# Kernel optimization log

Hardware: AMD Instinct MI355X
Metric: run time of the kernel (lower is better)

## Reference

```python
import jax, jax.numpy as jnp
import numpy as np

SIGMA = 1e-4
GAMMA = 1e-4
BG_COLOR = (1.0, 1.0, 1.0)
ZNEAR = 1.0
ZFAR = 100.0
EPS = 1e-10


def setup_inputs() -> dict:
    key = jax.random.key(0)
    ks = jax.random.split(key, 7)
    N, H, W, K = 4, 512, 512, 8
    F, V = 100000, 50000
    p2f = jax.random.randint(ks[0], (N, H, W, K), 0, F)
    bg = jax.random.uniform(ks[1], (N, H, W, K)) < 0.3
    pix_to_face = jnp.where(bg, -1, p2f)
    b = jax.random.uniform(ks[2], (N, H, W, K, 3)) + 1e-3
    bary_coords = b / b.sum(-1, keepdims=True)  # valid barycentric weights
    dists = jax.random.normal(ks[3], (N, H, W, K)) * 1e-4  # signed edge distances
    zbuf = ZNEAR + (ZFAR - ZNEAR) * jax.random.uniform(ks[4], (N, H, W, K))
    zbuf = jnp.sort(zbuf, axis=-1)  # rasterizer returns K faces sorted by depth
    faces = jax.random.randint(ks[5], (F, 3), 0, V)
    vn = jax.random.normal(ks[6], (V, 3))
    vertex_normals = vn / jnp.linalg.norm(vn, axis=-1, keepdims=True)
    return dict(pix_to_face=pix_to_face, bary_coords=bary_coords, dists=dists,
                zbuf=zbuf, faces=faces, vertex_normals=vertex_normals)


def reference(pix_to_face, bary_coords, dists, zbuf, faces, vertex_normals):
    # ---- interpolate_face_attributes ----
    mask = pix_to_face >= 0                              # (N,H,W,K)
    idx = jnp.where(mask, pix_to_face, 0)
    face_normals = vertex_normals[faces]                 # (F,3,3) gather verts per face
    attrs = face_normals[idx]                            # (N,H,W,K,3,3) irregular gather
    pixel_normals = jnp.einsum('nhwkv,nhwkvc->nhwkc', bary_coords, attrs)
    pixel_normals = jnp.where(mask[..., None], pixel_normals, 0.0)

    # ---- softmax_rgb_blend ----
    maskf = mask.astype(pixel_normals.dtype)
    prob_map = jax.nn.sigmoid(-dists / SIGMA) * maskf
    alpha = 1.0 - jnp.prod(1.0 - prob_map, axis=-1)      # (N,H,W)
    z_inv = (ZFAR - zbuf) / (ZFAR - ZNEAR) * maskf
    z_inv_max = jnp.maximum(jnp.max(z_inv, axis=-1, keepdims=True), EPS)
    weights_num = prob_map * jnp.exp((z_inv - z_inv_max) / GAMMA)
    delta = jnp.maximum(jnp.exp((EPS - z_inv_max[..., 0]) / GAMMA), EPS)  # (N,H,W)
    denom = weights_num.sum(-1) + delta                  # (N,H,W)
    weighted_colors = jnp.einsum('nhwk,nhwkc->nhwc', weights_num, pixel_normals)
    bg = jnp.asarray(BG_COLOR, dtype=pixel_normals.dtype)
    rgb = (weighted_colors + delta[..., None] * bg) / denom[..., None]
    return jnp.concatenate([rgb, alpha[..., None]], axis=-1)  # (N,H,W,4)
```

## Files before the change

kernel.cpp:

```cpp
#include <hip/hip_runtime.h>
#include <hip/hip_fp16.h>

#define SIGMA_F   1e-4f
#define GAMMA_F   1e-4f
#define ZNEAR_F   1.0f
#define ZFAR_F    100.0f
#define EPS_F     1e-10f

#define CULL_ARG  (-60.0f)

typedef float f32x4 __attribute__((ext_vector_type(4)));
typedef int   i32x4 __attribute__((ext_vector_type(4)));

struct __align__(16) H16 { __half h[16]; };

__global__ __launch_bounds__(256) void build_face_attrs(
    const int*   __restrict__ faces,
    const float* __restrict__ vnorm,
    H16*         __restrict__ attrs,
    int F)
{
    int f = blockIdx.x * blockDim.x + threadIdx.x;
    if (f >= F) return;
    int v0 = faces[(size_t)f * 3 + 0];
    int v1 = faces[(size_t)f * 3 + 1];
    int v2 = faces[(size_t)f * 3 + 2];

    H16 a;
    a.h[0] = __float2half(vnorm[(size_t)v0 * 3 + 0]);
    a.h[1] = __float2half(vnorm[(size_t)v0 * 3 + 1]);
    a.h[2] = __float2half(vnorm[(size_t)v0 * 3 + 2]);
    a.h[3] = __float2half(vnorm[(size_t)v1 * 3 + 0]);
    a.h[4] = __float2half(vnorm[(size_t)v1 * 3 + 1]);
    a.h[5] = __float2half(vnorm[(size_t)v1 * 3 + 2]);
    a.h[6] = __float2half(vnorm[(size_t)v2 * 3 + 0]);
    a.h[7] = __float2half(vnorm[(size_t)v2 * 3 + 1]);
    a.h[8] = __float2half(vnorm[(size_t)v2 * 3 + 2]);
    #pragma unroll
    for (int i = 9; i < 16; ++i) a.h[i] = __half(0.0f);
    attrs[f] = a;
}

__global__ __launch_bounds__(256) void shade_kernel(
    const int*   __restrict__ pix_to_face,
    const float* __restrict__ bary,
    const float* __restrict__ dists,
    const float* __restrict__ zbuf,
    const H16*   __restrict__ attrs,
    float*       __restrict__ out,
    int P)
{
    int pix = blockIdx.x * blockDim.x + threadIdx.x;
    if (pix >= P) return;

    const i32x4* p2f4 = reinterpret_cast<const i32x4*>(pix_to_face + (size_t)pix * 8);
    i32x4 f0 = __builtin_nontemporal_load(p2f4 + 0);
    i32x4 f1 = __builtin_nontemporal_load(p2f4 + 1);
    int faceid[8] = {f0.x, f0.y, f0.z, f0.w, f1.x, f1.y, f1.z, f1.w};

    const f32x4* d4 = reinterpret_cast<const f32x4*>(dists + (size_t)pix * 8);
    f32x4 da = __builtin_nontemporal_load(d4 + 0);
    f32x4 db = __builtin_nontemporal_load(d4 + 1);
    float dd[8] = {da.x, da.y, da.z, da.w, db.x, db.y, db.z, db.w};

    const f32x4* z4 = reinterpret_cast<const f32x4*>(zbuf + (size_t)pix * 8);
    f32x4 za = __builtin_nontemporal_load(z4 + 0);
    f32x4 zb = __builtin_nontemporal_load(z4 + 1);
    float zz[8] = {za.x, za.y, za.z, za.w, zb.x, zb.y, zb.z, zb.w};

    const float inv_sigma = 1.0f / SIGMA_F;
    const float inv_range = 1.0f / (ZFAR_F - ZNEAR_F);
    const float inv_gamma = 1.0f / GAMMA_F;

    float prob[8], zinv[8];
    float zmax = EPS_F;
    float one_minus_prod = 1.0f;

    #pragma unroll
    for (int k = 0; k < 8; ++k) {
        bool m = faceid[k] >= 0;
        float pm = 1.0f / (1.0f + __expf(dd[k] * inv_sigma));
        pm = m ? pm : 0.0f;
        prob[k] = pm;
        one_minus_prod *= (1.0f - pm);
        float zi = (ZFAR_F - zz[k]) * inv_range;
        zi = m ? zi : 0.0f;
        zinv[k] = zi;
        zmax = fmaxf(zmax, zi);
    }
    float alpha = 1.0f - one_minus_prod;

    int   k0 = 8, fsel = 0;
    float zsel = 0.0f, psel = 0.0f;
    #pragma unroll
    for (int k = 7; k >= 0; --k) {
        bool m = faceid[k] >= 0;
        k0   = m ? k          : k0;
        fsel = m ? faceid[k]  : fsel;
        zsel = m ? zinv[k]    : zsel;
        psel = m ? prob[k]    : psel;
    }

    bool ext[8];
    #pragma unroll
    for (int k = 0; k < 8; ++k)
        ext[k] = (faceid[k] >= 0) && ((zinv[k] - zmax) * inv_gamma > CULL_ARG) && (k != k0);

    int   k1 = 8, f1sel = 0;
    float z1 = 0.0f, p1 = 0.0f;
    #pragma unroll
    for (int k = 7; k >= 0; --k) {
        bool e = ext[k];
        k1    = e ? k         : k1;
        f1sel = e ? faceid[k] : f1sel;
        z1    = e ? zinv[k]   : z1;
        p1    = e ? prob[k]   : p1;
    }
    bool has1 = (k1 < 8);

    int ko0 = (k0 < 8) ? k0 : 0;
    int ko1 = has1 ? k1 : ko0;
    const float* bp = bary + (size_t)pix * 24;
    float a0 = bp[ko0 * 3 + 0], a1 = bp[ko0 * 3 + 1], a2 = bp[ko0 * 3 + 2];
    float c0 = bp[ko1 * 3 + 0], c1 = bp[ko1 * 3 + 1], c2 = bp[ko1 * 3 + 2];
    H16 g0 = attrs[fsel];
    H16 g1 = attrs[f1sel];

    float w0 = psel * __expf((zsel - zmax) * inv_gamma);
    float w1 = p1   * __expf((z1   - zmax) * inv_gamma);
    w1 = has1 ? w1 : 0.0f;

    float px0 = a0 * __half2float(g0.h[0]) + a1 * __half2float(g0.h[3]) + a2 * __half2float(g0.h[6]);
    float py0 = a0 * __half2float(g0.h[1]) + a1 * __half2float(g0.h[4]) + a2 * __half2float(g0.h[7]);
    float pz0 = a0 * __half2float(g0.h[2]) + a1 * __half2float(g0.h[5]) + a2 * __half2float(g0.h[8]);
    float px1 = c0 * __half2float(g1.h[0]) + c1 * __half2float(g1.h[3]) + c2 * __half2float(g1.h[6]);
    float py1 = c0 * __half2float(g1.h[1]) + c1 * __half2float(g1.h[4]) + c2 * __half2float(g1.h[7]);
    float pz1 = c0 * __half2float(g1.h[2]) + c1 * __half2float(g1.h[5]) + c2 * __half2float(g1.h[8]);

    float wsum = w0 + w1;
    float cr = w0 * px0 + w1 * px1;
    float cg = w0 * py0 + w1 * py1;
    float cb = w0 * pz0 + w1 * pz1;

    bool more = false;
    #pragma unroll
    for (int k = 0; k < 8; ++k) more |= (ext[k] && k != k1);
    if (__any(more)) {
        #pragma unroll
        for (int k = 0; k < 8; ++k) {
            if (ext[k] && k != k1) {
                float b0 = bp[k * 3 + 0], b1 = bp[k * 3 + 1], b2 = bp[k * 3 + 2];
                H16 g = attrs[faceid[k]];
                float w = prob[k] * __expf((zinv[k] - zmax) * inv_gamma);
                float px = b0 * __half2float(g.h[0]) + b1 * __half2float(g.h[3]) + b2 * __half2float(g.h[6]);
                float py = b0 * __half2float(g.h[1]) + b1 * __half2float(g.h[4]) + b2 * __half2float(g.h[7]);
                float pz = b0 * __half2float(g.h[2]) + b1 * __half2float(g.h[5]) + b2 * __half2float(g.h[8]);
                wsum += w;
                cr += w * px;
                cg += w * py;
                cb += w * pz;
            }
        }
    }

    float delta = fmaxf(__expf((EPS_F - zmax) * inv_gamma), EPS_F);
    float inv_denom = 1.0f / (wsum + delta);

    f32x4 o;
    o.x = (cr + delta) * inv_denom;
    o.y = (cg + delta) * inv_denom;
    o.z = (cb + delta) * inv_denom;
    o.w = alpha;
    __builtin_nontemporal_store(o, reinterpret_cast<f32x4*>(out) + pix);
}

__global__ __launch_bounds__(256) void normal_shader_fused(
    const int*   __restrict__ pix_to_face,
    const float* __restrict__ bary,
    const float* __restrict__ dists,
    const float* __restrict__ zbuf,
    const int*   __restrict__ faces,
    const float* __restrict__ vnorm,
    float*       __restrict__ out,
    int P)
{
    int pix = blockIdx.x * blockDim.x + threadIdx.x;
    if (pix >= P) return;

    const i32x4* p2f4 = reinterpret_cast<const i32x4*>(pix_to_face + (size_t)pix * 8);
    i32x4 f0 = p2f4[0], f1 = p2f4[1];
    int faceid[8] = {f0.x, f0.y, f0.z, f0.w, f1.x, f1.y, f1.z, f1.w};

    const f32x4* d4 = reinterpret_cast<const f32x4*>(dists + (size_t)pix * 8);
    f32x4 da = d4[0], db = d4[1];
    float dd[8] = {da.x, da.y, da.z, da.w, db.x, db.y, db.z, db.w};

    const f32x4* z4 = reinterpret_cast<const f32x4*>(zbuf + (size_t)pix * 8);
    f32x4 za = z4[0], zb = z4[1];
    float zz[8] = {za.x, za.y, za.z, za.w, zb.x, zb.y, zb.z, zb.w};

    const float inv_sigma = 1.0f / SIGMA_F;
    const float inv_range = 1.0f / (ZFAR_F - ZNEAR_F);
    const float inv_gamma = 1.0f / GAMMA_F;

    float prob[8], zinv[8];
    float zmax = EPS_F, one_minus_prod = 1.0f;

    #pragma unroll
    for (int k = 0; k < 8; ++k) {
        bool m = faceid[k] >= 0;
        float pm = 1.0f / (1.0f + __expf(dd[k] * inv_sigma));
        pm = m ? pm : 0.0f;
        prob[k] = pm;
        one_minus_prod *= (1.0f - pm);
        float zi = (ZFAR_F - zz[k]) * inv_range;
        zinv[k] = m ? zi : 0.0f;
        zmax = fmaxf(zmax, zinv[k]);
    }
    float alpha = 1.0f - one_minus_prod;

    int k0 = 8, fsel = 0; float zsel = 0.0f, psel = 0.0f;
    #pragma unroll
    for (int k = 7; k >= 0; --k) {
        bool m = faceid[k] >= 0;
        k0 = m ? k : k0; fsel = m ? faceid[k] : fsel;
        zsel = m ? zinv[k] : zsel; psel = m ? prob[k] : psel;
    }

    bool ext[8];
    #pragma unroll
    for (int k = 0; k < 8; ++k)
        ext[k] = (faceid[k] >= 0) && ((zinv[k] - zmax) * inv_gamma > CULL_ARG) && (k != k0);

    int k1 = 8, f1sel = 0; float z1 = 0.0f, p1 = 0.0f;
    #pragma unroll
    for (int k = 7; k >= 0; --k) {
        bool e = ext[k];
        k1 = e ? k : k1; f1sel = e ? faceid[k] : f1sel;
        z1 = e ? zinv[k] : z1; p1 = e ? prob[k] : p1;
    }
    bool has1 = (k1 < 8);

    int ko0 = (k0 < 8) ? k0 : 0;
    int ko1 = has1 ? k1 : ko0;
    const float* bp = bary + (size_t)pix * 24;
    float a0 = bp[ko0 * 3 + 0], a1 = bp[ko0 * 3 + 1], a2 = bp[ko0 * 3 + 2];
    float c0 = bp[ko1 * 3 + 0], c1 = bp[ko1 * 3 + 1], c2 = bp[ko1 * 3 + 2];

    int v00 = faces[(size_t)fsel * 3 + 0], v01 = faces[(size_t)fsel * 3 + 1], v02 = faces[(size_t)fsel * 3 + 2];
    int v10 = faces[(size_t)f1sel * 3 + 0], v11 = faces[(size_t)f1sel * 3 + 1], v12 = faces[(size_t)f1sel * 3 + 2];

    float w0 = psel * __expf((zsel - zmax) * inv_gamma);
    float w1 = p1 * __expf((z1 - zmax) * inv_gamma);
    w1 = has1 ? w1 : 0.0f;

    const float* n00 = vnorm + (size_t)v00 * 3;
    const float* n01 = vnorm + (size_t)v01 * 3;
    const float* n02 = vnorm + (size_t)v02 * 3;
    const float* n10 = vnorm + (size_t)v10 * 3;
    const float* n11 = vnorm + (size_t)v11 * 3;
    const float* n12 = vnorm + (size_t)v12 * 3;

    float px0 = a0 * n00[0] + a1 * n01[0] + a2 * n02[0];
    float py0 = a0 * n00[1] + a1 * n01[1] + a2 * n02[1];
    float pz0 = a0 * n00[2] + a1 * n01[2] + a2 * n02[2];
    float px1 = c0 * n10[0] + c1 * n11[0] + c2 * n12[0];
    float py1 = c0 * n10[1] + c1 * n11[1] + c2 * n12[1];
    float pz1 = c0 * n10[2] + c1 * n11[2] + c2 * n12[2];

    float wsum = w0 + w1;
    float cr = w0 * px0 + w1 * px1;
    float cg = w0 * py0 + w1 * py1;
    float cb = w0 * pz0 + w1 * pz1;

    bool more = false;
    #pragma unroll
    for (int k = 0; k < 8; ++k) more |= (ext[k] && k != k1);
    if (__any(more)) {
        #pragma unroll
        for (int k = 0; k < 8; ++k) {
            if (ext[k] && k != k1) {
                int fi = faceid[k];
                int u0 = faces[(size_t)fi * 3 + 0];
                int u1 = faces[(size_t)fi * 3 + 1];
                int u2 = faces[(size_t)fi * 3 + 2];
                float b0 = bp[k * 3 + 0], b1 = bp[k * 3 + 1], b2 = bp[k * 3 + 2];
                const float* m0 = vnorm + (size_t)u0 * 3;
                const float* m1 = vnorm + (size_t)u1 * 3;
                const float* m2 = vnorm + (size_t)u2 * 3;
                float w = prob[k] * __expf((zinv[k] - zmax) * inv_gamma);
                wsum += w;
                cr += w * (b0 * m0[0] + b1 * m1[0] + b2 * m2[0]);
                cg += w * (b0 * m0[1] + b1 * m1[1] + b2 * m2[1]);
                cb += w * (b0 * m0[2] + b1 * m1[2] + b2 * m2[2]);
            }
        }
    }

    float delta = fmaxf(__expf((EPS_F - zmax) * inv_gamma), EPS_F);
    float inv_denom = 1.0f / (wsum + delta);
    f32x4 o;
    o.x = (cr + delta) * inv_denom;
    o.y = (cg + delta) * inv_denom;
    o.z = (cb + delta) * inv_denom;
    o.w = alpha;
    reinterpret_cast<f32x4*>(out)[pix] = o;
}

extern "C" void kernel_launch(void* const* d_in, const int* in_sizes, int n_in,
                              void* d_out, int out_size, void* d_ws, size_t ws_size,
                              hipStream_t stream) {
    const int*   pix_to_face = (const int*)  d_in[0];
    const float* bary        = (const float*)d_in[1];
    const float* dists       = (const float*)d_in[2];
    const float* zbuf        = (const float*)d_in[3];
    const int*   faces       = (const int*)  d_in[4];
    const float* vnorm       = (const float*)d_in[5];
    float*       out         = (float*)d_out;

    int P = out_size / 4;
    int F = in_sizes[4] / 3;
    int block = 256;
    int gridP = (P + block - 1) / block;

    size_t attrs_bytes = (size_t)F * sizeof(H16);
    if (ws_size >= attrs_bytes) {
        H16* attrs = (H16*)d_ws;
        int gridF = (F + block - 1) / block;
        build_face_attrs<<<gridF, block, 0, stream>>>(faces, vnorm, attrs, F);
        shade_kernel<<<gridP, block, 0, stream>>>(
            pix_to_face, bary, dists, zbuf, attrs, out, P);
    } else {
        normal_shader_fused<<<gridP, block, 0, stream>>>(
            pix_to_face, bary, dists, zbuf, faces, vnorm, out, P);
    }
}
```

Baseline: 52.76 us.

## Process two pixels per thread with batched loads and split two-phase shading

The shading kernel now handles two pixels per thread. All streaming loads for both pixels are issued up front, then the first phase (probabilities, top-two selection, gathers) runs for both before the finish phase, which raises memory-level parallelism. The rare extra-face path no longer keeps per-k arrays live; it reloads and recomputes them from global memory, cutting register pressure so the launch bound can request 4 blocks. The cost is twice the work per thread, half as many blocks, and redundant reloads when the extra path is taken.

```diff
diff --git a/kernel.cpp b/kernel.cpp
--- a/kernel.cpp
+++ b/kernel.cpp
@@ -41,7 +41,162 @@
     attrs[f] = a;
 }
 
-__global__ __launch_bounds__(256) void shade_kernel(
+struct PixMid {
+    float a0, a1, a2, c0, c1, c2;
+    H16   g0, g1;
+    float w0, w1, alpha, zmax;
+    int   k0, k1;
+    int   pix;
+    bool  more, valid;
+};
+
+__device__ __forceinline__ PixMid pass1_px(
+    i32x4 F0, i32x4 F1, f32x4 DA, f32x4 DB, f32x4 ZA, f32x4 ZB,
+    int pix, bool valid,
+    const float* __restrict__ bary, const H16* __restrict__ attrs)
+{
+    int   faceid[8] = {F0.x, F0.y, F0.z, F0.w, F1.x, F1.y, F1.z, F1.w};
+    float dd[8]     = {DA.x, DA.y, DA.z, DA.w, DB.x, DB.y, DB.z, DB.w};
+    float zz[8]     = {ZA.x, ZA.y, ZA.z, ZA.w, ZB.x, ZB.y, ZB.z, ZB.w};
+
+    const float inv_sigma = 1.0f / SIGMA_F;
+    const float inv_range = 1.0f / (ZFAR_F - ZNEAR_F);
+    const float inv_gamma = 1.0f / GAMMA_F;
+
+    float prob[8], zinv[8];
+    float zmax = EPS_F, omp = 1.0f;
+    #pragma unroll
+    for (int k = 0; k < 8; ++k) {
+        bool m = faceid[k] >= 0;
+        float pm = 1.0f / (1.0f + __expf(dd[k] * inv_sigma));
+        pm = m ? pm : 0.0f;
+        prob[k] = pm;
+        omp *= (1.0f - pm);
+        float zi = (ZFAR_F - zz[k]) * inv_range;
+        zi = m ? zi : 0.0f;
+        zinv[k] = zi;
+        zmax = fmaxf(zmax, zi);
+    }
+
+    PixMid M;
+    M.alpha = 1.0f - omp;
+    M.zmax  = zmax;
+    M.pix   = pix;
+    M.valid = valid;
+
+    int k0 = 8, fsel = 0; float zsel = 0.0f, psel = 0.0f;
+    #pragma unroll
+    for (int k = 7; k >= 0; --k) {
+        bool m = faceid[k] >= 0;
+        k0 = m ? k : k0;  fsel = m ? faceid[k] : fsel;
+        zsel = m ? zinv[k] : zsel;  psel = m ? prob[k] : psel;
+    }
+
+    bool ext[8];
+    #pragma unroll
+    for (int k = 0; k < 8; ++k)
+        ext[k] = (faceid[k] >= 0) && ((zinv[k] - zmax) * inv_gamma > CULL_ARG) && (k != k0);
+
+    int k1 = 8, f1sel = 0; float z1 = 0.0f, p1 = 0.0f;
+    #pragma unroll
+    for (int k = 7; k >= 0; --k) {
+        bool e = ext[k];
+        k1 = e ? k : k1;  f1sel = e ? faceid[k] : f1sel;
+        z1 = e ? zinv[k] : z1;  p1 = e ? prob[k] : p1;
+    }
+    bool has1 = (k1 < 8);
+    M.k0 = k0;  M.k1 = k1;
+
+    bool more = false;
+    #pragma unroll
+    for (int k = 0; k < 8; ++k) more |= (ext[k] && k != k1);
+    M.more = more;
+
+    int ko0 = (k0 < 8) ? k0 : 0;
+    int ko1 = has1 ? k1 : ko0;
+    const float* bp = bary + (size_t)pix * 24;
+    M.a0 = bp[ko0 * 3 + 0];  M.a1 = bp[ko0 * 3 + 1];  M.a2 = bp[ko0 * 3 + 2];
+    M.c0 = bp[ko1 * 3 + 0];  M.c1 = bp[ko1 * 3 + 1];  M.c2 = bp[ko1 * 3 + 2];
+    M.g0 = attrs[fsel];
+    M.g1 = attrs[f1sel];
+
+    M.w0 = psel * __expf((zsel - zmax) * inv_gamma);
+    float w1 = p1 * __expf((z1 - zmax) * inv_gamma);
+    M.w1 = has1 ? w1 : 0.0f;
+    return M;
+}
+
+__device__ __forceinline__ void finish_px(
+    const PixMid& M,
+    const int*   __restrict__ pix_to_face,
+    const float* __restrict__ bary,
+    const float* __restrict__ dists,
+    const float* __restrict__ zbuf,
+    const H16*   __restrict__ attrs,
+    float*       __restrict__ out)
+{
+    const float inv_sigma = 1.0f / SIGMA_F;
+    const float inv_range = 1.0f / (ZFAR_F - ZNEAR_F);
+    const float inv_gamma = 1.0f / GAMMA_F;
+
+    float px0 = M.a0 * __half2float(M.g0.h[0]) + M.a1 * __half2float(M.g0.h[3]) + M.a2 * __half2float(M.g0.h[6]);
+    float py0 = M.a0 * __half2float(M.g0.h[1]) + M.a1 * __half2float(M.g0.h[4]) + M.a2 * __half2float(M.g0.h[7]);
+    float pz0 = M.a0 * __half2float(M.g0.h[2]) + M.a1 * __half2float(M.g0.h[5]) + M.a2 * __half2float(M.g0.h[8]);
+    float px1 = M.c0 * __half2float(M.g1.h[0]) + M.c1 * __half2float(M.g1.h[3]) + M.c2 * __half2float(M.g1.h[6]);
+    float py1 = M.c0 * __half2float(M.g1.h[1]) + M.c1 * __half2float(M.g1.h[4]) + M.c2 * __half2float(M.g1.h[7]);
+    float pz1 = M.c0 * __half2float(M.g1.h[2]) + M.c1 * __half2float(M.g1.h[5]) + M.c2 * __half2float(M.g1.h[8]);
+
+    float wsum = M.w0 + M.w1;
+    float cr = M.w0 * px0 + M.w1 * px1;
+    float cg = M.w0 * py0 + M.w1 * py1;
+    float cb = M.w0 * pz0 + M.w1 * pz1;
+
+    if (__any((int)M.more)) {
+        const i32x4* a4 = reinterpret_cast<const i32x4*>(pix_to_face + (size_t)M.pix * 8);
+        i32x4 F0 = a4[0], F1 = a4[1];
+        int fid[8] = {F0.x, F0.y, F0.z, F0.w, F1.x, F1.y, F1.z, F1.w};
+        const f32x4* d4 = reinterpret_cast<const f32x4*>(dists + (size_t)M.pix * 8);
+        f32x4 DA = d4[0], DB = d4[1];
+        float dd[8] = {DA.x, DA.y, DA.z, DA.w, DB.x, DB.y, DB.z, DB.w};
+        const f32x4* z4 = reinterpret_cast<const f32x4*>(zbuf + (size_t)M.pix * 8);
+        f32x4 ZA = z4[0], ZB = z4[1];
+        float zz[8] = {ZA.x, ZA.y, ZA.z, ZA.w, ZB.x, ZB.y, ZB.z, ZB.w};
+        const float* bp = bary + (size_t)M.pix * 24;
+
+        #pragma unroll
+        for (int k = 0; k < 8; ++k) {
+            bool m = fid[k] >= 0;
+            float pm = 1.0f / (1.0f + __expf(dd[k] * inv_sigma));
+            pm = m ? pm : 0.0f;
+            float zi = (ZFAR_F - zz[k]) * inv_range;
+            zi = m ? zi : 0.0f;
+            float arg = (zi - M.zmax) * inv_gamma;
+            bool e = m && (arg > CULL_ARG) && (k != M.k0) && (k != M.k1);
+            if (e) {
+                float b0 = bp[k * 3 + 0], b1 = bp[k * 3 + 1], b2 = bp[k * 3 + 2];
+                H16 g = attrs[fid[k]];
+                float w = pm * __expf(arg);
+                wsum += w;
+                cr += w * (b0 * __half2float(g.h[0]) + b1 * __half2float(g.h[3]) + b2 * __half2float(g.h[6]));
+                cg += w * (b0 * __half2float(g.h[1]) + b1 * __half2float(g.h[4]) + b2 * __half2float(g.h[7]));
+                cb += w * (b0 * __half2float(g.h[2]) + b1 * __half2float(g.h[5]) + b2 * __half2float(g.h[8]));
+            }
+        }
+    }
+
+    float delta = fmaxf(__expf((EPS_F - M.zmax) * inv_gamma), EPS_F);
+    float inv_denom = 1.0f / (wsum + delta);
+
+    f32x4 o;
+    o.x = (cr + delta) * inv_denom;
+    o.y = (cg + delta) * inv_denom;
+    o.z = (cb + delta) * inv_denom;
+    o.w = M.alpha;
+    if (M.valid)
+        __builtin_nontemporal_store(o, reinterpret_cast<f32x4*>(out) + M.pix);
+}
+
+__global__ __launch_bounds__(256, 4) void shade2_kernel(
     const int*   __restrict__ pix_to_face,
     const float* __restrict__ bary,
     const float* __restrict__ dists,
@@ -50,128 +205,40 @@
     float*       __restrict__ out,
     int P)
 {
-    int pix = blockIdx.x * blockDim.x + threadIdx.x;
-    if (pix >= P) return;
-
-    const i32x4* p2f4 = reinterpret_cast<const i32x4*>(pix_to_face + (size_t)pix * 8);
-    i32x4 f0 = __builtin_nontemporal_load(p2f4 + 0);
-    i32x4 f1 = __builtin_nontemporal_load(p2f4 + 1);
-    int faceid[8] = {f0.x, f0.y, f0.z, f0.w, f1.x, f1.y, f1.z, f1.w};
-
-    const f32x4* d4 = reinterpret_cast<const f32x4*>(dists + (size_t)pix * 8);
-    f32x4 da = __builtin_nontemporal_load(d4 + 0);
-    f32x4 db = __builtin_nontemporal_load(d4 + 1);
-    float dd[8] = {da.x, da.y, da.z, da.w, db.x, db.y, db.z, db.w};
-
-    const f32x4* z4 = reinterpret_cast<const f32x4*>(zbuf + (size_t)pix * 8);
-    f32x4 za = __builtin_nontemporal_load(z4 + 0);
-    f32x4 zb = __builtin_nontemporal_load(z4 + 1);
-    float zz[8] = {za.x, za.y, za.z, za.w, zb.x, zb.y, zb.z, zb.w};
-
-    const float inv_sigma = 1.0f / SIGMA_F;
-    const float inv_range = 1.0f / (ZFAR_F - ZNEAR_F);
-    const float inv_gamma = 1.0f / GAMMA_F;
-
-    float prob[8], zinv[8];
-    float zmax = EPS_F;
-    float one_minus_prod = 1.0f;
-
-    #pragma unroll
-    for (int k = 0; k < 8; ++k) {
-        bool m = faceid[k] >= 0;
-        float pm = 1.0f / (1.0f + __expf(dd[k] * inv_sigma));
-        pm = m ? pm : 0.0f;
-        prob[k] = pm;
-        one_minus_prod *= (1.0f - pm);
-        float zi = (ZFAR_F - zz[k]) * inv_range;
-        zi = m ? zi : 0.0f;
-        zinv[k] = zi;
-        zmax = fmaxf(zmax, zi);
-    }
-    float alpha = 1.0f - one_minus_prod;
-
-    int   k0 = 8, fsel = 0;
-    float zsel = 0.0f, psel = 0.0f;
-    #pragma unroll
-    for (int k = 7; k >= 0; --k) {
-        bool m = faceid[k] >= 0;
-        k0   = m ? k          : k0;
-        fsel = m ? faceid[k]  : fsel;
-        zsel = m ? zinv[k]    : zsel;
-        psel = m ? prob[k]    : psel;
-    }
-
-    bool ext[8];
-    #pragma unroll
-    for (int k = 0; k < 8; ++k)
-        ext[k] = (faceid[k] >= 0) && ((zinv[k] - zmax) * inv_gamma > CULL_ARG) && (k != k0);
-
-    int   k1 = 8, f1sel = 0;
-    float z1 = 0.0f, p1 = 0.0f;
-    #pragma unroll
-    for (int k = 7; k >= 0; --k) {
-        bool e = ext[k];
-        k1    = e ? k         : k1;
-        f1sel = e ? faceid[k] : f1sel;
-        z1    = e ? zinv[k]   : z1;
-        p1    = e ? prob[k]   : p1;
-    }
-    bool has1 = (k1 < 8);
-
-    int ko0 = (k0 < 8) ? k0 : 0;
-    int ko1 = has1 ? k1 : ko0;
-    const float* bp = bary + (size_t)pix * 24;
-    float a0 = bp[ko0 * 3 + 0], a1 = bp[ko0 * 3 + 1], a2 = bp[ko0 * 3 + 2];
-    float c0 = bp[ko1 * 3 + 0], c1 = bp[ko1 * 3 + 1], c2 = bp[ko1 * 3 + 2];
-    H16 g0 = attrs[fsel];
-    H16 g1 = attrs[f1sel];
-
-    float w0 = psel * __expf((zsel - zmax) * inv_gamma);
-    float w1 = p1   * __expf((z1   - zmax) * inv_gamma);
-    w1 = has1 ? w1 : 0.0f;
-
-    float px0 = a0 * __half2float(g0.h[0]) + a1 * __half2float(g0.h[3]) + a2 * __half2float(g0.h[6]);
-    float py0 = a0 * __half2float(g0.h[1]) + a1 * __half2float(g0.h[4]) + a2 * __half2float(g0.h[7]);
-    float pz0 = a0 * __half2float(g0.h[2]) + a1 * __half2float(g0.h[5]) + a2 * __half2float(g0.h[8]);
-    float px1 = c0 * __half2float(g1.h[0]) + c1 * __half2float(g1.h[3]) + c2 * __half2float(g1.h[6]);
-    float py1 = c0 * __half2float(g1.h[1]) + c1 * __half2float(g1.h[4]) + c2 * __half2float(g1.h[7]);
-    float pz1 = c0 * __half2float(g1.h[2]) + c1 * __half2float(g1.h[5]) + c2 * __half2float(g1.h[8]);
-
-    float wsum = w0 + w1;
-    float cr = w0 * px0 + w1 * px1;
-    float cg = w0 * py0 + w1 * py1;
-    float cb = w0 * pz0 + w1 * pz1;
-
-    bool more = false;
-    #pragma unroll
-    for (int k = 0; k < 8; ++k) more |= (ext[k] && k != k1);
-    if (__any(more)) {
-        #pragma unroll
-        for (int k = 0; k < 8; ++k) {
-            if (ext[k] && k != k1) {
-                float b0 = bp[k * 3 + 0], b1 = bp[k * 3 + 1], b2 = bp[k * 3 + 2];
-                H16 g = attrs[faceid[k]];
-                float w = prob[k] * __expf((zinv[k] - zmax) * inv_gamma);
-                float px = b0 * __half2float(g.h[0]) + b1 * __half2float(g.h[3]) + b2 * __half2float(g.h[6]);
-                float py = b0 * __half2float(g.h[1]) + b1 * __half2float(g.h[4]) + b2 * __half2float(g.h[7]);
-                float pz = b0 * __half2float(g.h[2]) + b1 * __half2float(g.h[5]) + b2 * __half2float(g.h[8]);
-                wsum += w;
-                cr += w * px;
-                cg += w * py;
-                cb += w * pz;
-            }
-        }
-    }
-
-    float delta = fmaxf(__expf((EPS_F - zmax) * inv_gamma), EPS_F);
-    float inv_denom = 1.0f / (wsum + delta);
-
-    f32x4 o;
-    o.x = (cr + delta) * inv_denom;
-    o.y = (cg + delta) * inv_denom;
-    o.z = (cb + delta) * inv_denom;
-    o.w = alpha;
-    __builtin_nontemporal_store(o, reinterpret_cast<f32x4*>(out) + pix);
+    int tid  = threadIdx.x;
+    int base = blockIdx.x * 512;
+
+    int pa = base + tid;
+    int pb = base + 256 + tid;
+    bool va = pa < P, vb = pb < P;
+    int qa = va ? pa : 0;
+    int qb = vb ? pb : 0;
+
+    const i32x4* a4 = reinterpret_cast<const i32x4*>(pix_to_face + (size_t)qa * 8);
+    i32x4 aF0 = __builtin_nontemporal_load(a4 + 0);
+    i32x4 aF1 = __builtin_nontemporal_load(a4 + 1);
+    const f32x4* ad4 = reinterpret_cast<const f32x4*>(dists + (size_t)qa * 8);
+    f32x4 aDA = __builtin_nontemporal_load(ad4 + 0);
+    f32x4 aDB = __builtin_nontemporal_load(ad4 + 1);
+    const f32x4* az4 = reinterpret_cast<const f32x4*>(zbuf + (size_t)qa * 8);
+    f32x4 aZA = __builtin_nontemporal_load(az4 + 0);
+    f32x4 aZB = __builtin_nontemporal_load(az4 + 1);
+
+    const i32x4* b4 = reinterpret_cast<const i32x4*>(pix_to_face + (size_t)qb * 8);
+    i32x4 bF0 = __builtin_nontemporal_load(b4 + 0);
+    i32x4 bF1 = __builtin_nontemporal_load(b4 + 1);
+    const f32x4* bd4 = reinterpret_cast<const f32x4*>(dists + (size_t)qb * 8);
+    f32x4 bDA = __builtin_nontemporal_load(bd4 + 0);
+    f32x4 bDB = __builtin_nontemporal_load(bd4 + 1);
+    const f32x4* bz4 = reinterpret_cast<const f32x4*>(zbuf + (size_t)qb * 8);
+    f32x4 bZA = __builtin_nontemporal_load(bz4 + 0);
+    f32x4 bZB = __builtin_nontemporal_load(bz4 + 1);
+
+    PixMid M0 = pass1_px(aF0, aF1, aDA, aDB, aZA, aZB, qa, va, bary, attrs);
+    PixMid M1 = pass1_px(bF0, bF1, bDA, bDB, bZA, bZB, qb, vb, bary, attrs);
+
+    finish_px(M0, pix_to_face, bary, dists, zbuf, attrs, out);
+    finish_px(M1, pix_to_face, bary, dists, zbuf, attrs, out);
 }
 
 __global__ __launch_bounds__(256) void normal_shader_fused(
@@ -276,7 +343,7 @@
     bool more = false;
     #pragma unroll
     for (int k = 0; k < 8; ++k) more |= (ext[k] && k != k1);
-    if (__any(more)) {
+    if (__any((int)more)) {
         #pragma unroll
         for (int k = 0; k < 8; ++k) {
             if (ext[k] && k != k1) {
@@ -321,16 +388,17 @@
     int P = out_size / 4;
     int F = in_sizes[4] / 3;
     int block = 256;
-    int gridP = (P + block - 1) / block;
 
     size_t attrs_bytes = (size_t)F * sizeof(H16);
     if (ws_size >= attrs_bytes) {
         H16* attrs = (H16*)d_ws;
         int gridF = (F + block - 1) / block;
         build_face_attrs<<<gridF, block, 0, stream>>>(faces, vnorm, attrs, F);
-        shade_kernel<<<gridP, block, 0, stream>>>(
+        int grid2 = (P + 511) / 512;
+        shade2_kernel<<<grid2, block, 0, stream>>>(
             pix_to_face, bary, dists, zbuf, attrs, out, P);
     } else {
+        int gridP = (P + block - 1) / block;
         normal_shader_fused<<<gridP, block, 0, stream>>>(
             pix_to_face, bary, dists, zbuf, faces, vnorm, out, P);
     }
```

Result: no change. 53.77 us (+1.9%).
